# Kernel tuning notes

Hardware: AMD Instinct MI355X
Metric: run time of the kernel (lower is better)

## Reference

```python
import jax, jax.numpy as jnp
import numpy as np

MAX_ROUNDS = 6
MIN_ROUNDS = 2
WINDOW = 4
LAMBDA_P = 0.2
LN_EPS = 1e-5


def _mlp(x, W1, b1, W2, b2):
    # Linear -> exact GELU -> Linear (matches nn.Sequential(Linear, GELU, Linear))
    return jax.nn.gelu(x @ W1 + b1, approximate=False) @ W2 + b2


def _layernorm(x, g, b):
    m = x.mean(-1, keepdims=True)
    v = x.var(-1, keepdims=True)
    return (x - m) / jnp.sqrt(v + LN_EPS) * g + b


def setup_inputs() -> dict:
    key = jax.random.key(0)
    ks = jax.random.split(key, 13)
    B, N, D = 4, 2048, 512
    s = 0.02
    f32 = jnp.float32
    return {
        "summaries": jax.random.normal(ks[0], (B, N, D), f32),
        "msg_W1": jax.random.normal(ks[1], (2 * D, D), f32) * s,
        "msg_b1": jnp.zeros((D,), f32),
        "msg_W2": jax.random.normal(ks[2], (D, D), f32) * s,
        "msg_b2": jnp.zeros((D,), f32),
        "upd_W1": jax.random.normal(ks[3], (2 * D, D), f32) * s,
        "upd_b1": jnp.zeros((D,), f32),
        "upd_W2": jax.random.normal(ks[4], (D, D), f32) * s,
        "upd_b2": jnp.zeros((D,), f32),
        "halt_W": jax.random.normal(ks[5], (D, 1), f32) * s,
        "halt_b": jnp.zeros((1,), f32),
        "ln_g": jnp.ones((D,), f32),
        "ln_b": jnp.zeros((D,), f32),
    }


def reference(summaries, msg_W1, msg_b1, msg_W2, msg_b2,
              upd_W1, upd_b1, upd_W2, upd_b2,
              halt_W, halt_b, ln_g, ln_b):
    B, N, D = summaries.shape
    dt = summaries.dtype
    h = summaries
    remaining = jnp.ones((B, N, 1), dt)
    output = jnp.zeros_like(h)
    kl = jnp.zeros((), dt)
    done = jnp.asarray(False)  # emulates the early `break` under jit
    pos = jnp.arange(N)
    # number of valid causal neighbors of position i: min(i+1, window+1)
    counts = jnp.minimum(pos + 1, WINDOW + 1).astype(dt)[None, :, None]

    for step in range(MAX_ROUNDS):
        # windowed gather + message MLP, vectorized over the (W+1) offsets
        acc = jnp.zeros_like(h)
        for d in range(WINDOW + 1):
            nb = h if d == 0 else jnp.pad(h, ((0, 0), (d, 0), (0, 0)))[:, :N]
            m = _mlp(jnp.concatenate([h, nb], axis=-1), msg_W1, msg_b1, msg_W2, msg_b2)
            mask = (pos >= d).astype(dt)[None, :, None]
            acc = acc + m * mask
        msgs = acc / counts  # mean over valid neighbors, shape (B, N, D)

        new_h = h + _mlp(jnp.concatenate([h, msgs], axis=-1), upd_W1, upd_b1, upd_W2, upd_b2)
        h_next = _layernorm(new_h, ln_g, ln_b)

        if step < MIN_ROUNDS:
            halt = jnp.zeros((B, N, 1), dt)
        elif step == MAX_ROUNDS - 1:
            halt = jnp.ones((B, N, 1), dt)
        else:
            hp = jax.nn.sigmoid(h_next.mean(axis=1, keepdims=True) @ halt_W + halt_b)  # (B,1,1)
            halt = jnp.broadcast_to(hp, (B, N, 1))

        step_weight = remaining * halt
        out_next = output + step_weight * h_next
        rem_next = remaining * (1.0 - halt)

        p_geom = LAMBDA_P * (1.0 - LAMBDA_P) ** step
        # F.kl_div(log(q), log(p), log_target=True) = p * (log p - log q)
        kl_term = p_geom * (jnp.log(p_geom) - jnp.log(halt.mean() + 1e-8))

        active = jnp.logical_not(done)
        af = active.astype(dt)
        h = jnp.where(active, h_next, h)
        output = jnp.where(active, out_next, output)
        remaining = jnp.where(active, rem_next, remaining)
        kl = kl + af * kl_term.astype(dt)
        done = jnp.logical_or(done, remaining.max() < 0.01)

    return output, kl / MAX_ROUNDS
```

## Files before the change

### kernel.cpp

```cpp
#include <hip/hip_runtime.h>
#include <cmath>

#define DEV __device__ __forceinline__

typedef __bf16 bf16x8 __attribute__((ext_vector_type(8)));
typedef float f32x4v __attribute__((ext_vector_type(4)));
typedef unsigned short u16x8 __attribute__((ext_vector_type(8)));
typedef unsigned short u16x4 __attribute__((ext_vector_type(4)));

DEV float bf2f(unsigned short u){ return __uint_as_float(((unsigned)u)<<16); }
DEV unsigned short f2bf(float f){
  unsigned u = __float_as_uint(f);
  u = (u + 0x7fffu + ((u>>16)&1u)) >> 16;
  return (unsigned short)u;
}
DEV float geluf(float x){
  const float z = fabsf(x) * 0.70710678118654752f;
  const float t = __builtin_amdgcn_rcpf(1.0f + 0.3275911f*z);
  const float p = t*(0.254829592f + t*(-0.284496736f + t*(1.421413741f
                + t*(-1.453152027f + t*1.061405429f))));
  float er = 1.0f - p*__expf(-z*z);
  er = (x < 0.0f) ? -er : er;
  return 0.5f*x*(1.0f + er);
}

#define GLDS16(g,l) __builtin_amdgcn_global_load_lds(\
    (const __attribute__((address_space(1))) void*)(g), \
    (__attribute__((address_space(3))) void*)(l), 16, 0, 0)

#define NB    4
#define NSEQ  2048
#define DDIM  512
#define MROWS 8192

#define OFF_H     0u
#define OFF_HB    16777216u
#define OFF_UV    25165824u
#define OFF_GP    25165824u
#define OFF_R     33554432u
#define OFF_GSC   41943040u
#define OFF_WUV   50331648u
#define OFF_WP    51380224u
#define OFF_WR    52428800u
#define OFF_BUV   52953088u
#define OFF_BP    52957184u
#define OFF_BR    52959232u
#define OFF_DOT   52961280u
#define OFF_SCAL  52994048u
#define OFF_FLAGS 52994112u
#define OFF_A2    25165824u
#define OFF_B2    25690112u

__global__ __launch_bounds__(256) void k_prep_tr(
    const float* __restrict__ mW1, const float* __restrict__ uW2,
    const float* __restrict__ uW1,
    unsigned short* __restrict__ Wuv, unsigned short* __restrict__ Wr,
    unsigned short* __restrict__ Wp,  unsigned short* __restrict__ A2)
{
  __shared__ float t[64][65];
  const int tid = threadIdx.x, c = tid&63, r4 = tid>>6;
  const float* src; unsigned short* dst; int dld;
  switch (blockIdx.y){
    case 0: src = mW1;          dst = Wuv;          dld = 512;  break;
    case 1: src = mW1 + 262144; dst = Wuv + 262144; dld = 512;  break;
    case 2: src = uW2;          dst = Wr;           dld = 512;  break;
    case 3: src = uW1;          dst = Wp;           dld = 1024; break;
    default:src = uW1 + 262144; dst = A2;           dld = 512;  break;
  }
  const int k0 = (blockIdx.x>>3)<<6, n0 = (blockIdx.x&7)<<6;
  #pragma unroll
  for (int i=0;i<16;++i){ int r = i*4 + r4; t[r][c] = src[(size_t)(k0+r)*512 + n0 + c]; }
  __syncthreads();
  #pragma unroll
  for (int i=0;i<16;++i){ int r = i*4 + r4; dst[(size_t)(n0+r)*dld + k0 + c] = f2bf(t[c][r]); }
}

__global__ __launch_bounds__(256) void k_prep_misc(
    const float* __restrict__ mW2, const float* __restrict__ mb1,
    const float* __restrict__ ub2, const float* __restrict__ ub1,
    const float* __restrict__ mb2, const float* __restrict__ uW1,
    unsigned short* __restrict__ B2, float* __restrict__ biasUV,
    float* __restrict__ biasR, float* __restrict__ biasP,
    float* __restrict__ scal, int* __restrict__ flags)
{
  const int bid = blockIdx.x, t = threadIdx.x;
  if (bid < 1024){
    int idx = bid*256 + t;
    B2[idx] = f2bf(mW2[idx]);
  } else if (bid == 1024){
    for (int i=t;i<1024;i+=256) biasUV[i] = (i<512)? mb1[i] : 0.f;
  } else if (bid == 1025){
    for (int i=t;i<512;i+=256) biasR[i] = ub2[i];
    if (t<4) scal[t]=1.f;
    else if (t<9) scal[t]=0.f;
    if (t==9){ flags[0]=1; flags[1]=0; }
  } else {
    int n = (bid-1026)*256 + t;
    float s = ub1[n];
    for (int j=0;j<512;++j) s += mb2[j]*uW1[(512+j)*512+n];
    biasP[n] = s;
  }
}

__global__ __launch_bounds__(256) void k_init_h(
    const float* __restrict__ S, float* __restrict__ H, u16x4* __restrict__ Hb)
{
  size_t idx = (size_t)blockIdx.x*256 + threadIdx.x;
  float4 v = ((const float4*)S)[idx];
  ((float4*)H)[idx] = v;
  u16x4 o; o[0]=f2bf(v.x); o[1]=f2bf(v.y); o[2]=f2bf(v.z); o[3]=f2bf(v.w);
  Hb[idx] = o;
}

template<int EPI>
__global__ __launch_bounds__(256) void k_gemm(
    const unsigned short* __restrict__ A0, const unsigned short* __restrict__ A1,
    const unsigned short* __restrict__ Bt, const float* __restrict__ bias,
    void* __restrict__ Cout, int ldc, int ldb, int nK, int ksplit, int gridN,
    const int* __restrict__ flags)
{
  if (flags[0]==0) return;
  __shared__ unsigned short sm[2][12288];
  const int tid = threadIdx.x;
  const int bid = blockIdx.x;
  const int nb  = (int)gridDim.x;
  const int ppx = (nb>>3)/gridN;
  int mp, np;
  if (ppx*gridN*8 == nb){ const int xcd = bid&7, ib = bid>>3; mp = xcd*ppx + ib/gridN; np = ib%gridN; }
  else                  { mp = bid/gridN; np = bid%gridN; }
  const int m0 = mp<<7, n0 = np<<6;
  const int sr = tid>>3;
  const int scA = (((tid&7) ^ (sr&7)) << 3);
  const int lane = tid&63, wv = tid>>6, wr = wv>>1, wc = wv&1;
  const int la = lane&15, lg = lane>>4;
  const int swzr = (la&7)<<3;
  f32x4v acc[4][2] = {};

  auto stage = [&](int ks, int bufi){
    const unsigned short* As = (ks<ksplit)? A0 : A1;
    const int kc = ((ks<ksplit)? ks : (ks-ksplit))<<6;
    unsigned short* s = sm[bufi];
    #pragma unroll
    for (int i=0;i<4;++i)
      GLDS16(As + (size_t)(m0 + i*32 + sr)*512 + kc + scA, s + i*2048 + tid*8);
    #pragma unroll
    for (int i=0;i<2;++i)
      GLDS16(Bt + (size_t)(n0 + i*32 + sr)*ldb + (ks<<6) + scA, s + 8192 + i*2048 + tid*8);
  };

  stage(0, 0);
  if (nK > 1) stage(1, 1);
  for (int ks=0; ks<nK; ++ks){
    const int cur = ks & 1;
    if (ks+1 < nK) asm volatile("s_waitcnt vmcnt(6)" ::: "memory");
    else           asm volatile("s_waitcnt vmcnt(0)" ::: "memory");
    __builtin_amdgcn_s_barrier();
    asm volatile("" ::: "memory");
    const unsigned short* s = sm[cur];
    #pragma unroll
    for (int kk=0;kk<2;++kk){
      bf16x8 af[4], bfr[2];
      #pragma unroll
      for (int mi=0;mi<4;++mi)
        af[mi] = *(const bf16x8*)(s + ((wr<<6) + (mi<<4) + la)*64 + (((kk<<5) + (lg<<3)) ^ swzr));
      #pragma unroll
      for (int ni=0;ni<2;++ni)
        bfr[ni] = *(const bf16x8*)(s + 8192 + ((wc<<5) + (ni<<4) + la)*64 + (((kk<<5) + (lg<<3)) ^ swzr));
      #pragma unroll
      for (int mi=0;mi<4;++mi)
        #pragma unroll
        for (int ni=0;ni<2;++ni)
          acc[mi][ni] = __builtin_amdgcn_mfma_f32_16x16x32_bf16(af[mi], bfr[ni], acc[mi][ni], 0, 0, 0);
    }
    asm volatile("" ::: "memory");
    __builtin_amdgcn_s_barrier();
    asm volatile("" ::: "memory");
    if (ks+2 < nK) stage(ks+2, cur);
  }

  const int r0 = m0 + (wr<<6) + (lg<<2);
  const int c0 = n0 + (wc<<5) + la;
  #pragma unroll
  for (int mi=0;mi<4;++mi){
    #pragma unroll
    for (int ni=0;ni<2;++ni){
      const int col = c0 + (ni<<4);
      const float bs = bias[col];
      #pragma unroll
      for (int r=0;r<4;++r){
        const int row = r0 + (mi<<4) + r;
        float v = acc[mi][ni][r] + bs;
        if constexpr (EPI==1) v = geluf(v);
        ((unsigned short*)Cout)[(size_t)row*ldc + col] = f2bf(v);
      }
    }
  }
}

__global__ __launch_bounds__(256) void k_geluacc(
    const unsigned short* __restrict__ UV, unsigned short* __restrict__ G,
    const int* __restrict__ flags)
{
  if (flags[0]==0) return;
  int r = blockIdx.x*4 + (threadIdx.x>>6);
  int lane = threadIdx.x & 63;
  int c8 = lane*8;
  int i = r & (NSEQ-1);
  int nd = (i<4) ? i : 4;
  const u16x8 u = *(const u16x8*)(UV + (size_t)r*1024 + c8);
  float acc[8] = {0,0,0,0,0,0,0,0};
  for (int d=0; d<=nd; ++d){
    const u16x8 v = *(const u16x8*)(UV + (size_t)(r-d)*1024 + 512 + c8);
    #pragma unroll
    for (int j=0;j<8;++j) acc[j] += geluf(bf2f(u[j]) + bf2f(v[j]));
  }
  float inv = 1.0f/(float)(nd+1);
  u16x8 o;
  #pragma unroll
  for (int j=0;j<8;++j) o[j] = f2bf(acc[j]*inv);
  *(u16x8*)(G + (size_t)r*512 + c8) = o;
}

__global__ __launch_bounds__(256) void k_ln(
    const unsigned short* __restrict__ Rr, float* __restrict__ H, unsigned short* __restrict__ Hb,
    const float* __restrict__ gamma, const float* __restrict__ beta,
    const float* __restrict__ hW, float* __restrict__ DOT, float* __restrict__ OUT,
    const float* __restrict__ scal, const int* __restrict__ flags,
    int accmode, int dodot)
{
  const int lane = threadIdx.x & 63;
  const int row = (blockIdx.x<<2) + (threadIdx.x>>6);
  const int bidx = row >> 11;
  const size_t base = (size_t)row*512 + lane*8;
  float4 x0 = *(const float4*)(H+base);
  float4 x1 = *(const float4*)(H+base+4);

  if (accmode){
    const float w = scal[4+bidx];
    float4 o0, o1;
    if (accmode==1){
      o0 = make_float4(w*x0.x, w*x0.y, w*x0.z, w*x0.w);
      o1 = make_float4(w*x1.x, w*x1.y, w*x1.z, w*x1.w);
    } else {
      o0 = *(const float4*)(OUT+base);
      o1 = *(const float4*)(OUT+base+4);
      o0.x += w*x0.x; o0.y += w*x0.y; o0.z += w*x0.z; o0.w += w*x0.w;
      o1.x += w*x1.x; o1.y += w*x1.y; o1.z += w*x1.z; o1.w += w*x1.w;
    }
    *(float4*)(OUT+base)   = o0;
    *(float4*)(OUT+base+4) = o1;
  }
  if (flags[0]==0) return;

  const u16x8 rv = *(const u16x8*)(Rr+base);
  x0.x+=bf2f(rv[0]); x0.y+=bf2f(rv[1]); x0.z+=bf2f(rv[2]); x0.w+=bf2f(rv[3]);
  x1.x+=bf2f(rv[4]); x1.y+=bf2f(rv[5]); x1.z+=bf2f(rv[6]); x1.w+=bf2f(rv[7]);
  float s = x0.x+x0.y+x0.z+x0.w + x1.x+x1.y+x1.z+x1.w;
  float q = x0.x*x0.x+x0.y*x0.y+x0.z*x0.z+x0.w*x0.w
          + x1.x*x1.x+x1.y*x1.y+x1.z*x1.z+x1.w*x1.w;
  #pragma unroll
  for (int off=1; off<64; off<<=1){ s += __shfl_xor(s, off); q += __shfl_xor(q, off); }
  const float mean = s*(1.f/512.f);
  const float var  = q*(1.f/512.f) - mean*mean;
  const float rstd = rsqrtf(var + 1e-5f);
  float4 g0 = *(const float4*)(gamma + lane*8);
  float4 g1 = *(const float4*)(gamma + lane*8 + 4);
  float4 b0 = *(const float4*)(beta  + lane*8);
  float4 b1 = *(const float4*)(beta  + lane*8 + 4);
  float y[8];
  y[0]=(x0.x-mean)*rstd*g0.x+b0.x; y[1]=(x0.y-mean)*rstd*g0.y+b0.y;
  y[2]=(x0.z-mean)*rstd*g0.z+b0.z; y[3]=(x0.w-mean)*rstd*g0.w+b0.w;
  y[4]=(x1.x-mean)*rstd*g1.x+b1.x; y[5]=(x1.y-mean)*rstd*g1.y+b1.y;
  y[6]=(x1.z-mean)*rstd*g1.z+b1.z; y[7]=(x1.w-mean)*rstd*g1.w+b1.w;
  *(float4*)(H+base)   = make_float4(y[0],y[1],y[2],y[3]);
  *(float4*)(H+base+4) = make_float4(y[4],y[5],y[6],y[7]);
  u16x8 hb;
  #pragma unroll
  for (int j=0;j<8;++j) hb[j] = f2bf(y[j]);
  *(u16x8*)(Hb+base) = hb;

  if (dodot){
    float4 w0 = *(const float4*)(hW + lane*8);
    float4 w1 = *(const float4*)(hW + lane*8 + 4);
    float d = y[0]*w0.x + y[1]*w0.y + y[2]*w0.z + y[3]*w0.w
            + y[4]*w1.x + y[5]*w1.y + y[6]*w1.z + y[7]*w1.w;
    #pragma unroll
    for (int off=1; off<64; off<<=1) d += __shfl_xor(d, off);
    if (lane==0) DOT[row] = d;
  }
}

__global__ void k_control(const float* __restrict__ DOT, const float* __restrict__ hb,
                          float* __restrict__ scal, int* __restrict__ flags,
                          int step, float p, float logp, float* __restrict__ klout)
{
  __shared__ float hp[4];
  const int t = threadIdx.x, lane = t&63, b = t>>6;
  if (step>=2 && step<5){
    float s = 0.f;
    for (int i=lane; i<NSEQ; i+=64) s += DOT[b*NSEQ + i];
    #pragma unroll
    for (int off=1; off<64; off<<=1) s += __shfl_xor(s, off);
    if (lane==0) hp[b] = s;
  } else if (lane==0) hp[b] = 0.f;
  __syncthreads();
  if (t==0){
    bool active = flags[0]!=0;
    float halt[NB];
    for (int i=0;i<NB;++i){
      if (step < 2) halt[i]=0.f;
      else if (step == 5) halt[i]=1.f;
      else { float z = hp[i]*(1.f/2048.f) + hb[0]; halt[i] = 1.f/(1.f+expf(-z)); }
    }
    float hm = 0.25f*(halt[0]+halt[1]+halt[2]+halt[3]);
    if (active) scal[8] += p*(logp - logf(hm + 1e-8f));
    float mx = 0.f;
    for (int i=0;i<NB;++i){
      float rb = scal[i];
      float w  = active ? rb*halt[i] : 0.f;
      scal[4+i] = w;
      if (active) rb *= (1.f - halt[i]);
      scal[i] = rb;
      mx = fmaxf(mx, rb);
    }
    if (mx < 0.01f) flags[1] = 1;
    flags[0] = flags[1] ? 0 : 1;
    if (step==5) *klout = scal[8]*(1.0f/6.0f);
  }
}

__global__ __launch_bounds__(256) void k_accum(
    const float* __restrict__ H, const float* __restrict__ scal, float* __restrict__ OUT)
{
  size_t idx = (size_t)blockIdx.x*256 + threadIdx.x;
  int b = (int)(idx >> 18);
  float w = scal[4+b];
  float4 h = ((const float4*)H)[idx];
  float4 o = ((float4*)OUT)[idx];
  ((float4*)OUT)[idx] = make_float4(o.x+w*h.x, o.y+w*h.y, o.z+w*h.z, o.w+w*h.w);
}

extern "C" void kernel_launch(void* const* d_in, const int* in_sizes, int n_in,
                              void* d_out, int out_size, void* d_ws, size_t ws_size,
                              hipStream_t stream)
{
  const float* S   = (const float*)d_in[0];
  const float* mW1 = (const float*)d_in[1];
  const float* mb1 = (const float*)d_in[2];
  const float* mW2 = (const float*)d_in[3];
  const float* mb2 = (const float*)d_in[4];
  const float* uW1 = (const float*)d_in[5];
  const float* ub1 = (const float*)d_in[6];
  const float* uW2 = (const float*)d_in[7];
  const float* ub2 = (const float*)d_in[8];
  const float* hW  = (const float*)d_in[9];
  const float* hb  = (const float*)d_in[10];
  const float* lng = (const float*)d_in[11];
  const float* lnb = (const float*)d_in[12];

  char* ws = (char*)d_ws;
  float*          H     = (float*)(ws + OFF_H);
  unsigned short* Hb    = (unsigned short*)(ws + OFF_HB);
  unsigned short* UV    = (unsigned short*)(ws + OFF_UV);
  unsigned short* GP    = (unsigned short*)(ws + OFF_GP);
  unsigned short* GSC   = (unsigned short*)(ws + OFF_GSC);
  unsigned short* Rb16  = (unsigned short*)(ws + OFF_R);
  unsigned short* Wuv   = (unsigned short*)(ws + OFF_WUV);
  unsigned short* Wp    = (unsigned short*)(ws + OFF_WP);
  unsigned short* Wr    = (unsigned short*)(ws + OFF_WR);
  unsigned short* A2    = (unsigned short*)(ws + OFF_A2);
  unsigned short* B2    = (unsigned short*)(ws + OFF_B2);
  float*          biasUV= (float*)(ws + OFF_BUV);
  float*          biasP = (float*)(ws + OFF_BP);
  float*          biasR = (float*)(ws + OFF_BR);
  float*          DOT   = (float*)(ws + OFF_DOT);
  float*          scal  = (float*)(ws + OFF_SCAL);
  int*            flags = (int*)(ws + OFF_FLAGS);
  float*          OUT   = (float*)d_out;
  float*          klout = OUT + (size_t)NB*NSEQ*DDIM;

  k_prep_tr  <<<dim3(64,5), 256, 0, stream>>>(mW1, uW2, uW1, Wuv, Wr, Wp, A2);
  k_prep_misc<<<1028, 256, 0, stream>>>(mW2, mb1, ub2, ub1, mb2, uW1,
                                        B2, biasUV, biasR, biasP, scal, flags);
  k_gemm<0><<<32, 256, 0, stream>>>(A2, A2, B2, biasUV+512, Wp+512, 1024, 512, 8, 8, 8, flags);
  k_init_h   <<<4096, 256, 0, stream>>>(S, H, (u16x4*)Hb);

  for (int s = 0; s < 6; ++s){
    k_gemm<0><<<1024, 256, 0, stream>>>(Hb, Hb, Wuv, biasUV, UV, 1024, 512, 8, 8, 16, flags);
    k_geluacc<<<2048, 256, 0, stream>>>(UV, GSC, flags);
    k_gemm<1><<<512, 256, 0, stream>>>(Hb, GSC, Wp, biasP, GP, 512, 1024, 16, 8, 8, flags);
    k_gemm<0><<<512, 256, 0, stream>>>(GP, GP, Wr, biasR, Rb16, 512, 512, 8, 8, 8, flags);
    const int accmode = (s==3) ? 1 : (s>=4 ? 2 : 0);
    const int dodot   = (s>=2 && s<=4) ? 1 : 0;
    k_ln<<<2048, 256, 0, stream>>>(Rb16, H, Hb, lng, lnb, hW, DOT, OUT, scal, flags, accmode, dodot);
    float p  = 0.2f * (float)pow(0.8, (double)s);
    float lp = (float)log((double)p);
    k_control<<<1, 256, 0, stream>>>(DOT, hb, scal, flags, s, p, lp, klout);
  }
  k_accum<<<4096, 256, 0, stream>>>(H, scal, OUT);
}
```

Before: 525.6 us.

## Use 128x128-tile GEMM for message projection and skip control launches for fixed-halt rounds

Adds a k_gemm128 kernel with 128x128 output tiles, 4x4 MFMA fragments per wave and double-buffered swizzled LDS staging, and uses it for the per-round H x Wuv projection in place of the 64-wide tile GEMM. Larger tiles raise data reuse per load and halve the block count. The control kernel is no longer launched for rounds 0 and 1, where halting is fixed at zero; their constant KL contribution is computed on the host and written into the scalar state at init. This removes two tiny serial launches, at the cost of more registers and LDS per block in the new GEMM.

```diff
diff --git a/kernel.cpp b/kernel.cpp
--- a/kernel.cpp
+++ b/kernel.cpp
@@ -81,7 +81,7 @@
     const float* __restrict__ mb2, const float* __restrict__ uW1,
     unsigned short* __restrict__ B2, float* __restrict__ biasUV,
     float* __restrict__ biasR, float* __restrict__ biasP,
-    float* __restrict__ scal, int* __restrict__ flags)
+    float* __restrict__ scal, int* __restrict__ flags, float kl01)
 {
   const int bid = blockIdx.x, t = threadIdx.x;
   if (bid < 1024){
@@ -92,7 +92,8 @@
   } else if (bid == 1025){
     for (int i=t;i<512;i+=256) biasR[i] = ub2[i];
     if (t<4) scal[t]=1.f;
-    else if (t<9) scal[t]=0.f;
+    else if (t<8) scal[t]=0.f;
+    if (t==8) scal[8]=kl01;
     if (t==9){ flags[0]=1; flags[1]=0; }
   } else {
     int n = (bid-1026)*256 + t;
@@ -192,6 +193,88 @@
         float v = acc[mi][ni][r] + bs;
         if constexpr (EPI==1) v = geluf(v);
         ((unsigned short*)Cout)[(size_t)row*ldc + col] = f2bf(v);
+      }
+    }
+  }
+}
+
+__global__ __launch_bounds__(256) void k_gemm128(
+    const unsigned short* __restrict__ A0,
+    const unsigned short* __restrict__ Bt, const float* __restrict__ bias,
+    unsigned short* __restrict__ Cout, int ldc, int ldb, int nK, int gridN,
+    const int* __restrict__ flags)
+{
+  if (flags[0]==0) return;
+  __shared__ unsigned short sm[2][16384];
+  const int tid = threadIdx.x;
+  const int bid = blockIdx.x;
+  const int nb  = (int)gridDim.x;
+  const int ppx = (nb>>3)/gridN;
+  int mp, np;
+  if (ppx*gridN*8 == nb){ const int xcd = bid&7, ib = bid>>3; mp = xcd*ppx + ib/gridN; np = ib%gridN; }
+  else                  { mp = bid/gridN; np = bid%gridN; }
+  const int m0 = mp<<7, n0 = np<<7;
+  const int sr = tid>>3;
+  const int scA = (((tid&7) ^ (sr&7)) << 3);
+  const int lane = tid&63, wv = tid>>6, wr = wv>>1, wc = wv&1;
+  const int la = lane&15, lg = lane>>4;
+  const int swzr = (la&7)<<3;
+  f32x4v acc[4][4] = {};
+
+  auto stage = [&](int ks, int bufi){
+    const int kc = ks<<6;
+    unsigned short* s = sm[bufi];
+    #pragma unroll
+    for (int i=0;i<4;++i)
+      GLDS16(A0 + (size_t)(m0 + i*32 + sr)*512 + kc + scA, s + i*2048 + tid*8);
+    #pragma unroll
+    for (int i=0;i<4;++i)
+      GLDS16(Bt + (size_t)(n0 + i*32 + sr)*ldb + kc + scA, s + 8192 + i*2048 + tid*8);
+  };
+
+  stage(0, 0);
+  if (nK > 1) stage(1, 1);
+  for (int ks=0; ks<nK; ++ks){
+    const int cur = ks & 1;
+    if (ks+1 < nK) asm volatile("s_waitcnt vmcnt(8)" ::: "memory");
+    else           asm volatile("s_waitcnt vmcnt(0)" ::: "memory");
+    __builtin_amdgcn_s_barrier();
+    asm volatile("" ::: "memory");
+    const unsigned short* s = sm[cur];
+    #pragma unroll
+    for (int kk=0;kk<2;++kk){
+      const int ko = ((kk<<5) + (lg<<3)) ^ swzr;
+      bf16x8 af[4], bfr[4];
+      #pragma unroll
+      for (int mi=0;mi<4;++mi)
+        af[mi] = *(const bf16x8*)(s + ((wr<<6) + (mi<<4) + la)*64 + ko);
+      #pragma unroll
+      for (int ni=0;ni<4;++ni)
+        bfr[ni] = *(const bf16x8*)(s + 8192 + ((wc<<6) + (ni<<4) + la)*64 + ko);
+      #pragma unroll
+      for (int mi=0;mi<4;++mi)
+        #pragma unroll
+        for (int ni=0;ni<4;++ni)
+          acc[mi][ni] = __builtin_amdgcn_mfma_f32_16x16x32_bf16(af[mi], bfr[ni], acc[mi][ni], 0, 0, 0);
+    }
+    asm volatile("" ::: "memory");
+    __builtin_amdgcn_s_barrier();
+    asm volatile("" ::: "memory");
+    if (ks+2 < nK) stage(ks+2, cur);
+  }
+
+  const int r0 = m0 + (wr<<6) + (lg<<2);
+  const int c0 = n0 + (wc<<6) + la;
+  #pragma unroll
+  for (int mi=0;mi<4;++mi){
+    #pragma unroll
+    for (int ni=0;ni<4;++ni){
+      const int col = c0 + (ni<<4);
+      const float bs = bias[col];
+      #pragma unroll
+      for (int r=0;r<4;++r){
+        const int row = r0 + (mi<<4) + r;
+        Cout[(size_t)row*ldc + col] = f2bf(acc[mi][ni][r] + bs);
       }
     }
   }
@@ -379,23 +462,28 @@
   float*          OUT   = (float*)d_out;
   float*          klout = OUT + (size_t)NB*NSEQ*DDIM;
 
+  const double lg8 = log(1e-8);
+  const float kl01 = (float)(0.2*(log(0.2)-lg8) + 0.16*(log(0.16)-lg8));
+
   k_prep_tr  <<<dim3(64,5), 256, 0, stream>>>(mW1, uW2, uW1, Wuv, Wr, Wp, A2);
   k_prep_misc<<<1028, 256, 0, stream>>>(mW2, mb1, ub2, ub1, mb2, uW1,
-                                        B2, biasUV, biasR, biasP, scal, flags);
+                                        B2, biasUV, biasR, biasP, scal, flags, kl01);
   k_gemm<0><<<32, 256, 0, stream>>>(A2, A2, B2, biasUV+512, Wp+512, 1024, 512, 8, 8, 8, flags);
   k_init_h   <<<4096, 256, 0, stream>>>(S, H, (u16x4*)Hb);
 
   for (int s = 0; s < 6; ++s){
-    k_gemm<0><<<1024, 256, 0, stream>>>(Hb, Hb, Wuv, biasUV, UV, 1024, 512, 8, 8, 16, flags);
+    k_gemm128<<<512, 256, 0, stream>>>(Hb, Wuv, biasUV, UV, 1024, 512, 8, 8, flags);
     k_geluacc<<<2048, 256, 0, stream>>>(UV, GSC, flags);
     k_gemm<1><<<512, 256, 0, stream>>>(Hb, GSC, Wp, biasP, GP, 512, 1024, 16, 8, 8, flags);
     k_gemm<0><<<512, 256, 0, stream>>>(GP, GP, Wr, biasR, Rb16, 512, 512, 8, 8, 8, flags);
     const int accmode = (s==3) ? 1 : (s>=4 ? 2 : 0);
     const int dodot   = (s>=2 && s<=4) ? 1 : 0;
     k_ln<<<2048, 256, 0, stream>>>(Rb16, H, Hb, lng, lnb, hW, DOT, OUT, scal, flags, accmode, dodot);
-    float p  = 0.2f * (float)pow(0.8, (double)s);
-    float lp = (float)log((double)p);
-    k_control<<<1, 256, 0, stream>>>(DOT, hb, scal, flags, s, p, lp, klout);
+    if (s >= 2){
+      float p  = 0.2f * (float)pow(0.8, (double)s);
+      float lp = (float)log((double)p);
+      k_control<<<1, 256, 0, stream>>>(DOT, hb, scal, flags, s, p, lp, klout);
+    }
   }
   k_accum<<<4096, 256, 0, stream>>>(H, scal, OUT);
 }
```

Result: faster. 506.8 us (-3.6%).
